# Optimization experiments

Hardware: AMD Instinct MI355X
Metric: run time of the kernel (lower is better)

Reference implementation:

```python
import jax, jax.numpy as jnp
import numpy as np


def gcn_conv(x, src, dst, W, b, num_nodes):
    # GCNConv: add self loops, sym-normalize by deg^{-1/2} on both ends.
    h = x @ W  # [N, out]
    loop = jnp.arange(num_nodes, dtype=src.dtype)
    s = jnp.concatenate([src, loop])
    d = jnp.concatenate([dst, loop])
    deg = jax.ops.segment_sum(jnp.ones(d.shape[0], dtype=h.dtype), d, num_segments=num_nodes)
    dinv = jax.lax.rsqrt(jnp.maximum(deg, 1.0))
    norm = dinv[s] * dinv[d]  # [E+N]
    out = jax.ops.segment_sum(h[s] * norm[:, None], d, num_segments=num_nodes)
    return out + b


def setup_inputs() -> dict:
    key = jax.random.key(0)
    ks = jax.random.split(key, 12)
    N, F, E, ED = 100000, 256, 1600000, 1000000
    x = jax.random.normal(ks[0], (N, F), jnp.float32)
    edge_index = jax.random.randint(ks[1], (2, E), 0, N, jnp.int32)
    total_edges = jax.random.randint(ks[2], (ED, 2), 0, N, jnp.int32)
    PI = jax.random.uniform(ks[3], (ED, 25), jnp.float32)
    W1 = jax.random.normal(ks[4], (F, 100), jnp.float32) * 0.05
    b1 = jnp.zeros((100,), jnp.float32)
    W2 = jax.random.normal(ks[5], (100, 16), jnp.float32) * 0.05
    b2 = jnp.zeros((16,), jnp.float32)
    lin1_W = jax.random.normal(ks[6], (41, 25), jnp.float32) * 0.05
    lin1_b = jnp.zeros((25,), jnp.float32)
    lin_W = jax.random.normal(ks[7], (25, 1), jnp.float32) * 0.05
    lin_b = jnp.zeros((1,), jnp.float32)
    return dict(x=x, edge_index=edge_index, total_edges=total_edges, PI=PI,
                W1=W1, b1=b1, W2=W2, b2=b2,
                lin1_W=lin1_W, lin1_b=lin1_b, lin_W=lin_W, lin_b=lin_b)


def reference(x, edge_index, total_edges, PI, W1, b1, W2, b2, lin1_W, lin1_b, lin_W, lin_b):
    N = x.shape[0]
    src, dst = edge_index[0], edge_index[1]
    # encode (eval mode: dropout is identity)
    h = jax.nn.relu(gcn_conv(x, src, dst, W1, b1, N))
    emb = jax.nn.relu(gcn_conv(h, src, dst, W2, b2, N))
    # renorm_(2, 0, 1): clamp each row's L2 norm to max 1
    nrm = jnp.linalg.norm(emb, axis=1, keepdims=True)
    emb = emb / jnp.maximum(nrm, 1.0)
    # decode: gather endpoint embeddings, squared diff, concat PI, small MLP
    emb_in = emb[total_edges[:, 0]]   # [ED, 16]
    emb_out = emb[total_edges[:, 1]]  # [ED, 16]
    sqdist = (emb_in - emb_out) ** 2  # [ED, 16]
    feat = jnp.concatenate([sqdist, PI], axis=1)  # [ED, 41]
    feat = jax.nn.leaky_relu(feat @ lin1_W + lin1_b, negative_slope=0.2)
    s = jnp.abs(feat @ lin_W + lin_b)[:, 0]
    s = jnp.clip(s, 0.0, 40.0)
    prob = jax.nn.sigmoid(2.0 - s)  # == 1/(exp(s-2)+1)
    return prob
```

## Files before the change

### kernel.cpp

```cpp
#include <hip/hip_runtime.h>
#include <hip/hip_bf16.h>
#include <math.h>

#define H1 100
#define H2 16
#define FDIM 256
#define NPAD 112
#define BINCH 4096

typedef __attribute__((ext_vector_type(8))) short bf16x8;
typedef __attribute__((ext_vector_type(4))) float f32x4;
typedef float f32x4a __attribute__((ext_vector_type(4), aligned(4)));

__device__ __forceinline__ float bf_lo(unsigned u) { return __uint_as_float(u << 16); }
__device__ __forceinline__ float bf_hi(unsigned u) { return __uint_as_float(u & 0xffff0000u); }
__device__ __forceinline__ unsigned f2bf_bits(float f) {
  unsigned x = __float_as_uint(f);
  return (x + 0x7fffu + ((x >> 16) & 1u)) >> 16;
}
__device__ __forceinline__ unsigned pack_bf16(float a, float b) {
  __hip_bfloat162 h = __float22bfloat162_rn(make_float2(a, b));
  unsigned u;
  __builtin_memcpy(&u, &h, 4);
  return u;
}

__global__ __launch_bounds__(256)
void k_bincnt(const int* __restrict__ dst, int* __restrict__ bucket_cnt,
              int E, int shift) {
  __shared__ int lcnt[512];
  int t = threadIdx.x;
  for (int i = t; i < 512; i += 256) lcnt[i] = 0;
  __syncthreads();
  int base = blockIdx.x * BINCH;
#pragma unroll
  for (int i = 0; i < 16; i++) {
    int e = base + t + i * 256;
    if (e < E) atomicAdd(&lcnt[dst[e] >> shift], 1);
  }
  __syncthreads();
  for (int b = t; b < 512; b += 256) {
    int c = lcnt[b];
    if (c > 0) atomicAdd(&bucket_cnt[b], c);
  }
}

__global__ void k_bscan(const int* __restrict__ bucket_cnt, int* __restrict__ bucket_base,
                        int* __restrict__ bucket_fill, int nbuc, int E) {
  __shared__ int s[512];
  int tid = threadIdx.x;
  int v = (tid < nbuc) ? bucket_cnt[tid] : 0;
  s[tid] = v;
  __syncthreads();
  for (int off = 1; off < 512; off <<= 1) {
    int tt = (tid >= off) ? s[tid - off] : 0;
    __syncthreads();
    s[tid] += tt;
    __syncthreads();
  }
  if (tid < nbuc) { int ex = s[tid] - v; bucket_base[tid] = ex; bucket_fill[tid] = ex; }
  if (tid == 0) bucket_base[nbuc] = E;
}

__global__ __launch_bounds__(256)
void k_binwrite(const int* __restrict__ src, const int* __restrict__ dst,
                int* __restrict__ bucket_fill, int2* __restrict__ tpair,
                int E, int shift) {
  __shared__ int lcnt[512];
  __shared__ int loff[512];
  int t = threadIdx.x;
  for (int i = t; i < 512; i += 256) lcnt[i] = 0;
  __syncthreads();
  int base = blockIdx.x * BINCH;
  int d[16], s_[16];
#pragma unroll
  for (int i = 0; i < 16; i++) {
    int e = base + t + i * 256;
    if (e < E) {
      d[i] = dst[e]; s_[i] = src[e];
      atomicAdd(&lcnt[d[i] >> shift], 1);
    } else d[i] = -1;
  }
  __syncthreads();
  for (int b = t; b < 512; b += 256) {
    int c = lcnt[b];
    loff[b] = (c > 0) ? atomicAdd(&bucket_fill[b], c) : 0;
  }
  __syncthreads();
#pragma unroll
  for (int i = 0; i < 16; i++) {
    if (d[i] >= 0) {
      int p = atomicAdd(&loff[d[i] >> shift], 1);
      tpair[p] = make_int2(d[i], s_[i]);
    }
  }
}

__global__ __launch_bounds__(256)
void k_deg2(const int2* __restrict__ tpair, const int* __restrict__ bucket_base,
            int* __restrict__ deg, float* __restrict__ dinv, int N, int shift) {
  __shared__ int lcnt[1024];
  int b = blockIdx.x, t = threadIdx.x;
  int bs = 1 << shift, mask = bs - 1;
  for (int i = t; i < bs; i += 256) lcnt[i] = 0;
  __syncthreads();
  int r0 = bucket_base[b], r1 = bucket_base[b + 1];
  for (int e = r0 + t; e < r1; e += 256) atomicAdd(&lcnt[tpair[e].x & mask], 1);
  __syncthreads();
  for (int i = t; i < bs; i += 256) {
    int node = (b << shift) + i;
    if (node < N) {
      deg[node] = lcnt[i];
      dinv[node] = rsqrtf((float)(lcnt[i] + 1));
    }
  }
}

__global__ __launch_bounds__(256)
void k_csr2(const int2* __restrict__ tpair,
            const int* __restrict__ bucket_base, const int* __restrict__ row_ptr,
            int* __restrict__ col_src, int N, int shift) {
  __shared__ int lrp[1024];
  __shared__ int lfill[1024];
  int b = blockIdx.x, t = threadIdx.x;
  int bs = 1 << shift, mask = bs - 1;
  for (int i = t; i < bs; i += 256) {
    int node = (b << shift) + i;
    lrp[i] = row_ptr[node < N ? node : N];
    lfill[i] = 0;
  }
  __syncthreads();
  int r0 = bucket_base[b], r1 = bucket_base[b + 1];
  for (int e = r0 + t; e < r1; e += 256) {
    int2 pr = tpair[e];
    int dl = pr.x & mask;
    int p = lrp[dl] + atomicAdd(&lfill[dl], 1);
    col_src[p] = pr.y;
  }
}

__global__ void k_scanA(const int* __restrict__ deg, int* __restrict__ row_ptr,
                        int* __restrict__ psum, int n) {
  __shared__ int s[256];
  int tid = threadIdx.x;
  int i = blockIdx.x * 256 + tid;
  int v = (i < n) ? deg[i] : 0;
  s[tid] = v;
  __syncthreads();
  for (int off = 1; off < 256; off <<= 1) {
    int t = (tid >= off) ? s[tid - off] : 0;
    __syncthreads();
    s[tid] += t;
    __syncthreads();
  }
  if (i < n) row_ptr[i] = s[tid] - v;
  if (tid == 255) psum[blockIdx.x] = s[255];
}

__global__ void k_scanB(int* psum, int nb) {
  __shared__ int s[512];
  int tid = threadIdx.x;
  int v = (tid < nb) ? psum[tid] : 0;
  s[tid] = v;
  __syncthreads();
  for (int off = 1; off < 512; off <<= 1) {
    int t = (tid >= off) ? s[tid - off] : 0;
    __syncthreads();
    s[tid] += t;
    __syncthreads();
  }
  if (tid < nb) psum[tid] = s[tid] - v;
}

__global__ void k_scanC(int* row_ptr, const int* __restrict__ psum, int n, int E) {
  int i = blockIdx.x * blockDim.x + threadIdx.x;
  if (i < n) row_ptr[i] += psum[i >> 8];
  if (i == 0) row_ptr[n] = E;
}

__global__ void k_w1cast(const float* __restrict__ W1, unsigned short* __restrict__ W1bf) {
  int i = blockIdx.x * 256 + threadIdx.x;
  if (i >= NPAD * FDIM) return;
  int col = i / FDIM, k = i % FDIM;
  float v = (col < H1) ? W1[k * H1 + col] : 0.f;
  W1bf[i] = (unsigned short)f2bf_bits(v);
}

__global__ __launch_bounds__(512, 2)
void k_gemm1m(const float* __restrict__ x, const unsigned short* __restrict__ W1bf,
              const float* __restrict__ dinv, unsigned short* __restrict__ t1p, int n) {
  __shared__ unsigned short ws[NPAD * FDIM];
  int tid = threadIdx.x;
  int lane = tid & 63, w = tid >> 6;
  int lr = lane & 15, lg = lane >> 4;
  int r0 = blockIdx.x * 128 + w * 16;
  int arow = r0 + lr;
  const float* xrow = x + (size_t)(arow < n ? arow : 0) * FDIM;

  float4 va[16];
#pragma unroll
  for (int s = 0; s < 8; ++s) {
    int kb = s * 32 + lg * 8;
    va[2 * s]     = *(const float4*)(xrow + kb);
    va[2 * s + 1] = *(const float4*)(xrow + kb + 4);
  }

  for (int i = tid; i < NPAD * FDIM / 8; i += 512) {
    int col = i >> 5;
    int kc = i & 31;
    uint4 v = *(const uint4*)(W1bf + col * FDIM + kc * 8);
    unsigned addr = (unsigned)(col * 512 + kc * 16) ^ ((unsigned)(col & 7) << 4);
    *(uint4*)((char*)ws + addr) = v;
  }
  asm volatile("" ::: "memory");
  __syncthreads();

  bf16x8 af[8];
#pragma unroll
  for (int s = 0; s < 8; ++s) {
    uint4 au;
    au.x = pack_bf16(va[2 * s].x, va[2 * s].y);
    au.y = pack_bf16(va[2 * s].z, va[2 * s].w);
    au.z = pack_bf16(va[2 * s + 1].x, va[2 * s + 1].y);
    au.w = pack_bf16(va[2 * s + 1].z, va[2 * s + 1].w);
    af[s] = *(bf16x8*)&au;
  }

  f32x4 acc[7];
#pragma unroll
  for (int nt = 0; nt < 7; nt++) acc[nt] = (f32x4){0.f, 0.f, 0.f, 0.f};

#pragma unroll
  for (int s = 0; s < 8; ++s) {
    int kb = s * 32 + lg * 8;
#pragma unroll
    for (int nt = 0; nt < 7; nt++) {
      int col = nt * 16 + lr;
      unsigned addr = (unsigned)(col * 512 + kb * 2) ^ ((unsigned)(col & 7) << 4);
      bf16x8 b = *(bf16x8*)((char*)ws + addr);
      acc[nt] = __builtin_amdgcn_mfma_f32_16x16x32_bf16(af[s], b, acc[nt], 0, 0, 0);
    }
  }

  float dv[4];
  int rbase = r0 + lg * 4;
#pragma unroll
  for (int r = 0; r < 4; r++) dv[r] = (rbase + r < n) ? dinv[rbase + r] : 0.f;
#pragma unroll
  for (int nt = 0; nt < 7; nt++) {
    int col = nt * 16 + lr;
    if (col < H1) {
#pragma unroll
      for (int r = 0; r < 4; r++) {
        int row = rbase + r;
        if (row < n)
          t1p[(size_t)row * H1 + col] = (unsigned short)f2bf_bits(acc[nt][r] * dv[r]);
      }
    }
  }
}

__global__ __launch_bounds__(256)
void k_agg1(const unsigned* __restrict__ t1p, const int* __restrict__ row_ptr,
            const int* __restrict__ col_src, const float* __restrict__ dinv,
            const float* __restrict__ b1, unsigned* __restrict__ h, int n) {
  int wv = __builtin_amdgcn_readfirstlane((int)(threadIdx.x >> 6));
  int wid = blockIdx.x * 4 + wv;
  if (wid >= n) return;
  int lane = threadIdx.x & 63;
  if (lane >= 50) return;
  int beg = row_ptr[wid], end = row_ptr[wid + 1];
  float a0 = 0.f, a1 = 0.f;
  int e = beg;
  for (; e + 8 <= end; e += 8) {
    int s0 = col_src[e + 0], s1 = col_src[e + 1];
    int s2 = col_src[e + 2], s3 = col_src[e + 3];
    int s4 = col_src[e + 4], s5 = col_src[e + 5];
    int s6 = col_src[e + 6], s7 = col_src[e + 7];
    unsigned u0 = t1p[(size_t)s0 * 50 + lane];
    unsigned u1 = t1p[(size_t)s1 * 50 + lane];
    unsigned u2 = t1p[(size_t)s2 * 50 + lane];
    unsigned u3 = t1p[(size_t)s3 * 50 + lane];
    unsigned u4 = t1p[(size_t)s4 * 50 + lane];
    unsigned u5 = t1p[(size_t)s5 * 50 + lane];
    unsigned u6 = t1p[(size_t)s6 * 50 + lane];
    unsigned u7 = t1p[(size_t)s7 * 50 + lane];
    a0 += bf_lo(u0); a1 += bf_hi(u0);
    a0 += bf_lo(u1); a1 += bf_hi(u1);
    a0 += bf_lo(u2); a1 += bf_hi(u2);
    a0 += bf_lo(u3); a1 += bf_hi(u3);
    a0 += bf_lo(u4); a1 += bf_hi(u4);
    a0 += bf_lo(u5); a1 += bf_hi(u5);
    a0 += bf_lo(u6); a1 += bf_hi(u6);
    a0 += bf_lo(u7); a1 += bf_hi(u7);
  }
  int rem = end - e;
  if (rem > 0) {
    int last = end - 1;
    int i1 = (e + 1 < end) ? e + 1 : last;
    int i2 = (e + 2 < end) ? e + 2 : last;
    int i3 = (e + 3 < end) ? e + 3 : last;
    int i4 = (e + 4 < end) ? e + 4 : last;
    int i5 = (e + 5 < end) ? e + 5 : last;
    int i6 = (e + 6 < end) ? e + 6 : last;
    int i7 = (e + 7 < end) ? e + 7 : last;
    int s0 = col_src[e],  s1 = col_src[i1], s2 = col_src[i2], s3 = col_src[i3];
    int s4 = col_src[i4], s5 = col_src[i5], s6 = col_src[i6], s7 = col_src[i7];
    unsigned u0 = t1p[(size_t)s0 * 50 + lane];
    unsigned u1 = (rem > 1) ? t1p[(size_t)s1 * 50 + lane] : 0u;
    unsigned u2 = (rem > 2) ? t1p[(size_t)s2 * 50 + lane] : 0u;
    unsigned u3 = (rem > 3) ? t1p[(size_t)s3 * 50 + lane] : 0u;
    unsigned u4 = (rem > 4) ? t1p[(size_t)s4 * 50 + lane] : 0u;
    unsigned u5 = (rem > 5) ? t1p[(size_t)s5 * 50 + lane] : 0u;
    unsigned u6 = (rem > 6) ? t1p[(size_t)s6 * 50 + lane] : 0u;
    unsigned u7 = 0u;
    (void)s7; (void)u7;
    a0 += bf_lo(u0); a1 += bf_hi(u0);
    a0 += bf_lo(u1); a1 += bf_hi(u1);
    a0 += bf_lo(u2); a1 += bf_hi(u2);
    a0 += bf_lo(u3); a1 += bf_hi(u3);
    a0 += bf_lo(u4); a1 += bf_hi(u4);
    a0 += bf_lo(u5); a1 += bf_hi(u5);
    a0 += bf_lo(u6); a1 += bf_hi(u6);
  }
  unsigned su = t1p[(size_t)wid * 50 + lane];
  a0 += bf_lo(su);
  a1 += bf_hi(su);
  float dv = dinv[wid];
  float v0 = fmaxf(dv * a0 + b1[2 * lane], 0.f);
  float v1 = fmaxf(dv * a1 + b1[2 * lane + 1], 0.f);
  h[(size_t)wid * 50 + lane] = pack_bf16(v0, v1);
}

__global__ __launch_bounds__(256)
void k_gemm2(const unsigned* __restrict__ h, const float* __restrict__ W2,
             const float* __restrict__ dinv, unsigned* __restrict__ t2p, int n) {
  __shared__ alignas(16) float w2s[100][16];
  __shared__ float hs[64][101];
  int tid = threadIdx.x;
  int r0 = blockIdx.x * 64;
  for (int idx = tid; idx < H1 * H2; idx += 256) w2s[idx / 16][idx % 16] = W2[idx];
  for (int idx = tid; idx < 64 * 50; idx += 256) {
    int row = idx / 50, u = idx % 50;
    int gr = r0 + row;
    unsigned v = 0;
    if (gr < n) v = h[(size_t)gr * 50 + u];
    hs[row][2 * u + 0] = bf_lo(v);
    hs[row][2 * u + 1] = bf_hi(v);
  }
  __syncthreads();
  int r = tid & 63, cg = tid >> 6;
  float ax = 0.f, ay = 0.f, az = 0.f, aw = 0.f;
#pragma unroll 4
  for (int k = 0; k < H1; ++k) {
    float a = hs[r][k];
    float4 w = *(const float4*)&w2s[k][cg * 4];
    ax += a * w.x; ay += a * w.y; az += a * w.z; aw += a * w.w;
  }
  int gr = r0 + r;
  if (gr < n) {
    float dv = dinv[gr];
    unsigned u0 = pack_bf16(ax * dv, ay * dv);
    unsigned u1 = pack_bf16(az * dv, aw * dv);
    *(uint2*)(t2p + (size_t)gr * 8 + cg * 2) = make_uint2(u0, u1);
  }
}

__global__ __launch_bounds__(256)
void k_agg2(const unsigned* __restrict__ t2p, const int* __restrict__ row_ptr,
            const int* __restrict__ col_src, const float* __restrict__ dinv,
            const float* __restrict__ b2, float* __restrict__ emb, int n) {
  int wv = __builtin_amdgcn_readfirstlane((int)(threadIdx.x >> 6));
  int wid = blockIdx.x * 4 + wv;
  if (wid >= n) return;
  int lane = threadIdx.x & 63;
  int es = lane >> 3, c = lane & 7;
  int beg = row_ptr[wid], end = row_ptr[wid + 1];
  float a0 = 0.f, a1 = 0.f;
  for (int e = beg + es; e < end; e += 8) {
    int s = col_src[e];
    unsigned u = t2p[(size_t)s * 8 + c];
    a0 += bf_lo(u);
    a1 += bf_hi(u);
  }
  a0 += __shfl_xor(a0, 8, 64);  a1 += __shfl_xor(a1, 8, 64);
  a0 += __shfl_xor(a0, 16, 64); a1 += __shfl_xor(a1, 16, 64);
  a0 += __shfl_xor(a0, 32, 64); a1 += __shfl_xor(a1, 32, 64);
  unsigned su = t2p[(size_t)wid * 8 + c];
  a0 += bf_lo(su);
  a1 += bf_hi(su);
  float dv = dinv[wid];
  float v0 = fmaxf(dv * a0 + b2[2 * c + 0], 0.f);
  float v1 = fmaxf(dv * a1 + b2[2 * c + 1], 0.f);
  float n2 = v0 * v0 + v1 * v1;
  n2 += __shfl_xor(n2, 1, 64);
  n2 += __shfl_xor(n2, 2, 64);
  n2 += __shfl_xor(n2, 4, 64);
  float scale = 1.f / fmaxf(sqrtf(n2), 1.f);
  if (es == 0) {
    *(float2*)(emb + (size_t)wid * H2 + 2 * c) = make_float2(v0 * scale, v1 * scale);
  }
}

__global__ void k_sprep(const float* __restrict__ l1W, uint4* __restrict__ Bt) {
  int lane = threadIdx.x;
  int lr = lane & 15, lg = lane >> 4;
  float wb[16];
#pragma unroll
  for (int i = 0; i < 8; i++) {
    int k0 = lg * 8 + i;
    wb[i] = (lr < 25) ? l1W[k0 * 25 + lr] : 0.f;
    int k1 = 32 + lg * 8 + i;
    wb[8 + i] = (lr < 25 && k1 < 41) ? l1W[k1 * 25 + lr] : 0.f;
  }
  int j1 = 16 + lr;
  float wb2[16];
#pragma unroll
  for (int i = 0; i < 8; i++) {
    int k0 = lg * 8 + i;
    wb2[i] = (j1 < 25) ? l1W[k0 * 25 + j1] : 0.f;
    int k1 = 32 + lg * 8 + i;
    wb2[8 + i] = (j1 < 25 && k1 < 41) ? l1W[k1 * 25 + j1] : 0.f;
  }
  uint4 B00, B01, B10, B11;
  B00.x = pack_bf16(wb[0], wb[1]);  B00.y = pack_bf16(wb[2], wb[3]);
  B00.z = pack_bf16(wb[4], wb[5]);  B00.w = pack_bf16(wb[6], wb[7]);
  B01.x = pack_bf16(wb[8], wb[9]);  B01.y = pack_bf16(wb[10], wb[11]);
  B01.z = pack_bf16(wb[12], wb[13]); B01.w = pack_bf16(wb[14], wb[15]);
  B10.x = pack_bf16(wb2[0], wb2[1]); B10.y = pack_bf16(wb2[2], wb2[3]);
  B10.z = pack_bf16(wb2[4], wb2[5]); B10.w = pack_bf16(wb2[6], wb2[7]);
  B11.x = pack_bf16(wb2[8], wb2[9]); B11.y = pack_bf16(wb2[10], wb2[11]);
  B11.z = pack_bf16(wb2[12], wb2[13]); B11.w = pack_bf16(wb2[14], wb2[15]);
  Bt[lane * 4 + 0] = B00;
  Bt[lane * 4 + 1] = B01;
  Bt[lane * 4 + 2] = B10;
  Bt[lane * 4 + 3] = B11;
}

__global__ __launch_bounds__(256)
void k_score(const float* __restrict__ emb, const int* __restrict__ te,
             const float* __restrict__ PI, const uint4* __restrict__ Bt,
             const float* __restrict__ l1b, const float* __restrict__ lW,
             const float* __restrict__ lb, float* __restrict__ out, int ned) {
  int tid = threadIdx.x;
  int lane = tid & 63, w = tid >> 6;
  int lr = lane & 15, lg = lane >> 4;
  int e0 = blockIdx.x * 128 + w * 32;
  int ea = e0 + lr, eb = e0 + 16 + lr;
  int eca = (ea < ned) ? ea : 0;
  int ecb = (eb < ned) ? eb : 0;

  uint4 B00 = Bt[lane * 4 + 0];
  uint4 B01 = Bt[lane * 4 + 1];
  uint4 B10 = Bt[lane * 4 + 2];
  uint4 B11 = Bt[lane * 4 + 3];

  const float* pia = PI + (size_t)eca * 25;
  const float* pib = PI + (size_t)ecb * 25;

  uint4 A0a = {0u,0u,0u,0u}, A1a = {0u,0u,0u,0u};
  uint4 A0b = {0u,0u,0u,0u}, A1b = {0u,0u,0u,0u};

  if (lg < 2) {
    int2 uva = *(const int2*)(te + 2 * (size_t)eca);
    int2 uvb = *(const int2*)(te + 2 * (size_t)ecb);
    const float* eua = emb + (size_t)uva.x * H2 + lg * 8;
    const float* eva = emb + (size_t)uva.y * H2 + lg * 8;
    const float* eub = emb + (size_t)uvb.x * H2 + lg * 8;
    const float* evb = emb + (size_t)uvb.y * H2 + lg * 8;
    float4 a0a = *(const float4*)(eua);
    float4 a1a = *(const float4*)(eua + 4);
    float4 b0a = *(const float4*)(eva);
    float4 b1a = *(const float4*)(eva + 4);
    float4 a0b = *(const float4*)(eub);
    float4 a1b = *(const float4*)(eub + 4);
    float4 b0b = *(const float4*)(evb);
    float4 b1b = *(const float4*)(evb + 4);
    {
      float d0 = a0a.x - b0a.x, d1 = a0a.y - b0a.y, d2 = a0a.z - b0a.z, d3 = a0a.w - b0a.w;
      float d4 = a1a.x - b1a.x, d5 = a1a.y - b1a.y, d6 = a1a.z - b1a.z, d7 = a1a.w - b1a.w;
      A0a.x = pack_bf16(d0 * d0, d1 * d1);
      A0a.y = pack_bf16(d2 * d2, d3 * d3);
      A0a.z = pack_bf16(d4 * d4, d5 * d5);
      A0a.w = pack_bf16(d6 * d6, d7 * d7);
    }
    {
      float d0 = a0b.x - b0b.x, d1 = a0b.y - b0b.y, d2 = a0b.z - b0b.z, d3 = a0b.w - b0b.w;
      float d4 = a1b.x - b1b.x, d5 = a1b.y - b1b.y, d6 = a1b.z - b1b.z, d7 = a1b.w - b1b.w;
      A0b.x = pack_bf16(d0 * d0, d1 * d1);
      A0b.y = pack_bf16(d2 * d2, d3 * d3);
      A0b.z = pack_bf16(d4 * d4, d5 * d5);
      A0b.w = pack_bf16(d6 * d6, d7 * d7);
    }
    if (lg == 0) {
      f32x4a pa0 = *(const f32x4a*)(pia + 16);
      f32x4a pa1 = *(const f32x4a*)(pia + 20);
      f32x4a pb0 = *(const f32x4a*)(pib + 16);
      f32x4a pb1 = *(const f32x4a*)(pib + 20);
      A1a.x = pack_bf16(pa0[0], pa0[1]); A1a.y = pack_bf16(pa0[2], pa0[3]);
      A1a.z = pack_bf16(pa1[0], pa1[1]); A1a.w = pack_bf16(pa1[2], pa1[3]);
      A1b.x = pack_bf16(pb0[0], pb0[1]); A1b.y = pack_bf16(pb0[2], pb0[3]);
      A1b.z = pack_bf16(pb1[0], pb1[1]); A1b.w = pack_bf16(pb1[2], pb1[3]);
    } else {
      A1a.x = pack_bf16(pia[24], 0.f);
      A1b.x = pack_bf16(pib[24], 0.f);
    }
  } else {
    const float* ppa = pia + (lg - 2) * 8;
    const float* ppb = pib + (lg - 2) * 8;
    f32x4a pa0 = *(const f32x4a*)(ppa);
    f32x4a pa1 = *(const f32x4a*)(ppa + 4);
    f32x4a pb0 = *(const f32x4a*)(ppb);
    f32x4a pb1 = *(const f32x4a*)(ppb + 4);
    A0a.x = pack_bf16(pa0[0], pa0[1]); A0a.y = pack_bf16(pa0[2], pa0[3]);
    A0a.z = pack_bf16(pa1[0], pa1[1]); A0a.w = pack_bf16(pa1[2], pa1[3]);
    A0b.x = pack_bf16(pb0[0], pb0[1]); A0b.y = pack_bf16(pb0[2], pb0[3]);
    A0b.z = pack_bf16(pb1[0], pb1[1]); A0b.w = pack_bf16(pb1[2], pb1[3]);
  }

  f32x4 acc0a = {0.f,0.f,0.f,0.f}, acc1a = {0.f,0.f,0.f,0.f};
  f32x4 acc0b = {0.f,0.f,0.f,0.f}, acc1b = {0.f,0.f,0.f,0.f};
  acc0a = __builtin_amdgcn_mfma_f32_16x16x32_bf16(*(bf16x8*)&A0a, *(bf16x8*)&B00, acc0a, 0, 0, 0);
  acc0b = __builtin_amdgcn_mfma_f32_16x16x32_bf16(*(bf16x8*)&A0b, *(bf16x8*)&B00, acc0b, 0, 0, 0);
  acc0a = __builtin_amdgcn_mfma_f32_16x16x32_bf16(*(bf16x8*)&A1a, *(bf16x8*)&B01, acc0a, 0, 0, 0);
  acc0b = __builtin_amdgcn_mfma_f32_16x16x32_bf16(*(bf16x8*)&A1b, *(bf16x8*)&B01, acc0b, 0, 0, 0);
  acc1a = __builtin_amdgcn_mfma_f32_16x16x32_bf16(*(bf16x8*)&A0a, *(bf16x8*)&B10, acc1a, 0, 0, 0);
  acc1b = __builtin_amdgcn_mfma_f32_16x16x32_bf16(*(bf16x8*)&A0b, *(bf16x8*)&B10, acc1b, 0, 0, 0);
  acc1a = __builtin_amdgcn_mfma_f32_16x16x32_bf16(*(bf16x8*)&A1a, *(bf16x8*)&B11, acc1a, 0, 0, 0);
  acc1b = __builtin_amdgcn_mfma_f32_16x16x32_bf16(*(bf16x8*)&A1b, *(bf16x8*)&B11, acc1b, 0, 0, 0);

  int j1 = 16 + lr;
  float bj0 = l1b[lr];
  float wj0 = lW[lr];
  float bj1 = (j1 < 25) ? l1b[j1] : 0.f;
  float wj1 = (j1 < 25) ? lW[j1] : 0.f;
  float lbv = lb[0];

  float pa[4], pb[4];
#pragma unroll
  for (int r = 0; r < 4; r++) {
    float x0 = acc0a[r] + bj0;
    x0 = (x0 > 0.f) ? x0 : 0.2f * x0;
    float x1 = acc1a[r] + bj1;
    x1 = (x1 > 0.f) ? x1 : 0.2f * x1;
    pa[r] = x0 * wj0 + ((j1 < 25) ? x1 * wj1 : 0.f);
    float y0 = acc0b[r] + bj0;
    y0 = (y0 > 0.f) ? y0 : 0.2f * y0;
    float y1 = acc1b[r] + bj1;
    y1 = (y1 > 0.f) ? y1 : 0.2f * y1;
    pb[r] = y0 * wj0 + ((j1 < 25) ? y1 * wj1 : 0.f);
  }
#pragma unroll
  for (int r = 0; r < 4; r++) {
    pa[r] += __shfl_xor(pa[r], 1, 64);
    pb[r] += __shfl_xor(pb[r], 1, 64);
    pa[r] += __shfl_xor(pa[r], 2, 64);
    pb[r] += __shfl_xor(pb[r], 2, 64);
    pa[r] += __shfl_xor(pa[r], 4, 64);
    pb[r] += __shfl_xor(pb[r], 4, 64);
    pa[r] += __shfl_xor(pa[r], 8, 64);
    pb[r] += __shfl_xor(pb[r], 8, 64);
  }
  if (lr == 0) {
#pragma unroll
    for (int r = 0; r < 4; r++) {
      int eoa = e0 + lg * 4 + r;
      if (eoa < ned) {
        float s = fminf(fabsf(pa[r] + lbv), 40.f);
        out[eoa] = 1.f / (1.f + __expf(-(2.f - s)));
      }
      int eob = e0 + 16 + lg * 4 + r;
      if (eob < ned) {
        float s = fminf(fabsf(pb[r] + lbv), 40.f);
        out[eob] = 1.f / (1.f + __expf(-(2.f - s)));
      }
    }
  }
}

extern "C" void kernel_launch(void* const* d_in, const int* in_sizes, int n_in,
                              void* d_out, int out_size, void* d_ws, size_t ws_size,
                              hipStream_t stream) {
  const float* x   = (const float*)d_in[0];
  const int*   ei  = (const int*)d_in[1];
  const int*   te  = (const int*)d_in[2];
  const float* PI  = (const float*)d_in[3];
  const float* W1  = (const float*)d_in[4];
  const float* b1  = (const float*)d_in[5];
  const float* W2  = (const float*)d_in[6];
  const float* b2  = (const float*)d_in[7];
  const float* l1W = (const float*)d_in[8];
  const float* l1b = (const float*)d_in[9];
  const float* lW  = (const float*)d_in[10];
  const float* lb  = (const float*)d_in[11];
  float* out = (float*)d_out;

  int h1 = in_sizes[5];
  int F  = in_sizes[4] / h1;
  int N  = in_sizes[0] / F;
  int E  = in_sizes[1] / 2;
  int ED = in_sizes[2] / 2;

  const int* src  = ei;
  const int* dstp = ei + E;

  int shift = 8;
  while ((((size_t)N + ((size_t)1 << shift) - 1) >> shift) > 512) shift++;
  int nbuc = (N + (1 << shift) - 1) >> shift;

  size_t off = 0;
  auto alloc = [&](size_t bytes) -> void* {
    void* p = (char*)d_ws + off;
    off += (bytes + 255) & ~(size_t)255;
    return p;
  };
  int*            deg      = (int*)alloc((size_t)N * 4);
  float*          dinv     = (float*)alloc((size_t)N * 4);
  int*            row_ptr  = (int*)alloc((size_t)(N + 1) * 4);
  int*            psum     = (int*)alloc(512 * 4);
  int*            bcnt     = (int*)alloc(512 * 4);
  int*            bbase    = (int*)alloc(520 * 4);
  int*            bfill    = (int*)alloc(512 * 4);
  int*            col_src  = (int*)alloc((size_t)E * 4);
  unsigned short* W1bf     = (unsigned short*)alloc((size_t)NPAD * FDIM * 2);
  uint4*          Bt       = (uint4*)alloc(64 * 4 * 16);
  unsigned*       t1p      = (unsigned*)alloc((size_t)N * 50 * 4 + 256);
  unsigned*       h        = (unsigned*)alloc((size_t)N * 50 * 4);
  unsigned*       t2p      = (unsigned*)alloc((size_t)N * 8 * 4);
  float*          emb      = (float*)alloc((size_t)N * H2 * 4);

  int2* tpair = (int2*)h;

  int nb = (N + 255) / 256;
  int nwb = (E + BINCH - 1) / BINCH;

  hipMemsetAsync(bcnt, 0, 512 * 4, stream);
  k_bincnt<<<nwb, 256, 0, stream>>>(dstp, bcnt, E, shift);
  k_bscan<<<1, 512, 0, stream>>>(bcnt, bbase, bfill, nbuc, E);
  k_binwrite<<<nwb, 256, 0, stream>>>(src, dstp, bfill, tpair, E, shift);
  k_deg2<<<nbuc, 256, 0, stream>>>(tpair, bbase, deg, dinv, N, shift);
  k_scanA<<<nb, 256, 0, stream>>>(deg, row_ptr, psum, N);
  k_scanB<<<1, 512, 0, stream>>>(psum, nb);
  k_scanC<<<nb, 256, 0, stream>>>(row_ptr, psum, N, E);
  k_csr2<<<nbuc, 256, 0, stream>>>(tpair, bbase, row_ptr, col_src, N, shift);
  k_w1cast<<<(NPAD * FDIM + 255) / 256, 256, 0, stream>>>(W1, W1bf);
  k_sprep<<<1, 64, 0, stream>>>(l1W, Bt);
  k_gemm1m<<<(N + 127) / 128, 512, 0, stream>>>(x, W1bf, dinv, (unsigned short*)t1p, N);
  k_agg1<<<(int)(((size_t)N * 64 + 255) / 256), 256, 0, stream>>>(t1p, row_ptr, col_src, dinv, b1, h, N);
  k_gemm2<<<(N + 63) / 64, 256, 0, stream>>>(h, W2, dinv, t2p, N);
  k_agg2<<<(int)(((size_t)N * 64 + 255) / 256), 256, 0, stream>>>(t2p, row_ptr, col_src, dinv, b2, emb, N);
  k_score<<<(ED + 127) / 128, 256, 0, stream>>>(emb, te, PI, Bt, l1b, lW, lb, out, ED);
}
```

Before: 285.7 us.

## Fuse degree and row-pointer scan per bucket; store embeddings as bf16

The per-bucket degree kernel now also computes an in-block exclusive scan and writes row_ptr directly, offset by the bucket base. This replaces the three-kernel global scan and removes the deg buffer. Separately, the normalized embeddings are stored as packed bf16, halving the random gather traffic in the scoring kernel, at some precision cost before the squared difference. A serial fallback path handles bucket sizes other than 256.

```diff
diff --git a/kernel.cpp b/kernel.cpp
--- a/kernel.cpp
+++ b/kernel.cpp
@@ -23,6 +23,11 @@
   unsigned u;
   __builtin_memcpy(&u, &h, 4);
   return u;
+}
+__device__ __forceinline__ unsigned sqd_pair(unsigned u, unsigned v) {
+  float d0 = bf_lo(u) - bf_lo(v);
+  float d1 = bf_hi(u) - bf_hi(v);
+  return pack_bf16(d0 * d0, d1 * d1);
 }
 
 __global__ __launch_bounds__(256)
@@ -97,9 +102,11 @@
 }
 
 __global__ __launch_bounds__(256)
-void k_deg2(const int2* __restrict__ tpair, const int* __restrict__ bucket_base,
-            int* __restrict__ deg, float* __restrict__ dinv, int N, int shift) {
+void k_deg2s(const int2* __restrict__ tpair, const int* __restrict__ bucket_base,
+             float* __restrict__ dinv, int* __restrict__ row_ptr,
+             int N, int E, int shift) {
   __shared__ int lcnt[1024];
+  __shared__ int lscan[256];
   int b = blockIdx.x, t = threadIdx.x;
   int bs = 1 << shift, mask = bs - 1;
   for (int i = t; i < bs; i += 256) lcnt[i] = 0;
@@ -107,11 +114,34 @@
   int r0 = bucket_base[b], r1 = bucket_base[b + 1];
   for (int e = r0 + t; e < r1; e += 256) atomicAdd(&lcnt[tpair[e].x & mask], 1);
   __syncthreads();
-  for (int i = t; i < bs; i += 256) {
-    int node = (b << shift) + i;
+  if (bs == 256) {
+    int v = lcnt[t];
+    lscan[t] = v;
+    __syncthreads();
+    for (int off = 1; off < 256; off <<= 1) {
+      int tt = (t >= off) ? lscan[t - off] : 0;
+      __syncthreads();
+      lscan[t] += tt;
+      __syncthreads();
+    }
+    int node = (b << shift) + t;
     if (node < N) {
-      deg[node] = lcnt[i];
-      dinv[node] = rsqrtf((float)(lcnt[i] + 1));
+      row_ptr[node] = r0 + lscan[t] - v;
+      dinv[node] = rsqrtf((float)(v + 1));
+      if (node == N - 1) row_ptr[N] = E;
+    }
+  } else {
+    if (t == 0) {
+      int acc = r0;
+      for (int i = 0; i < bs; i++) {
+        int node = (b << shift) + i;
+        if (node < N) {
+          row_ptr[node] = acc;
+          dinv[node] = rsqrtf((float)(lcnt[i] + 1));
+          if (node == N - 1) row_ptr[N] = E;
+        }
+        acc += lcnt[i];
+      }
     }
   }
 }
@@ -137,45 +167,6 @@
     int p = lrp[dl] + atomicAdd(&lfill[dl], 1);
     col_src[p] = pr.y;
   }
-}
-
-__global__ void k_scanA(const int* __restrict__ deg, int* __restrict__ row_ptr,
-                        int* __restrict__ psum, int n) {
-  __shared__ int s[256];
-  int tid = threadIdx.x;
-  int i = blockIdx.x * 256 + tid;
-  int v = (i < n) ? deg[i] : 0;
-  s[tid] = v;
-  __syncthreads();
-  for (int off = 1; off < 256; off <<= 1) {
-    int t = (tid >= off) ? s[tid - off] : 0;
-    __syncthreads();
-    s[tid] += t;
-    __syncthreads();
-  }
-  if (i < n) row_ptr[i] = s[tid] - v;
-  if (tid == 255) psum[blockIdx.x] = s[255];
-}
-
-__global__ void k_scanB(int* psum, int nb) {
-  __shared__ int s[512];
-  int tid = threadIdx.x;
-  int v = (tid < nb) ? psum[tid] : 0;
-  s[tid] = v;
-  __syncthreads();
-  for (int off = 1; off < 512; off <<= 1) {
-    int t = (tid >= off) ? s[tid - off] : 0;
-    __syncthreads();
-    s[tid] += t;
-    __syncthreads();
-  }
-  if (tid < nb) psum[tid] = s[tid] - v;
-}
-
-__global__ void k_scanC(int* row_ptr, const int* __restrict__ psum, int n, int E) {
-  int i = blockIdx.x * blockDim.x + threadIdx.x;
-  if (i < n) row_ptr[i] += psum[i >> 8];
-  if (i == 0) row_ptr[n] = E;
 }
 
 __global__ void k_w1cast(const float* __restrict__ W1, unsigned short* __restrict__ W1bf) {
@@ -303,9 +294,8 @@
     int i4 = (e + 4 < end) ? e + 4 : last;
     int i5 = (e + 5 < end) ? e + 5 : last;
     int i6 = (e + 6 < end) ? e + 6 : last;
-    int i7 = (e + 7 < end) ? e + 7 : last;
     int s0 = col_src[e],  s1 = col_src[i1], s2 = col_src[i2], s3 = col_src[i3];
-    int s4 = col_src[i4], s5 = col_src[i5], s6 = col_src[i6], s7 = col_src[i7];
+    int s4 = col_src[i4], s5 = col_src[i5], s6 = col_src[i6];
     unsigned u0 = t1p[(size_t)s0 * 50 + lane];
     unsigned u1 = (rem > 1) ? t1p[(size_t)s1 * 50 + lane] : 0u;
     unsigned u2 = (rem > 2) ? t1p[(size_t)s2 * 50 + lane] : 0u;
@@ -313,8 +303,6 @@
     unsigned u4 = (rem > 4) ? t1p[(size_t)s4 * 50 + lane] : 0u;
     unsigned u5 = (rem > 5) ? t1p[(size_t)s5 * 50 + lane] : 0u;
     unsigned u6 = (rem > 6) ? t1p[(size_t)s6 * 50 + lane] : 0u;
-    unsigned u7 = 0u;
-    (void)s7; (void)u7;
     a0 += bf_lo(u0); a1 += bf_hi(u0);
     a0 += bf_lo(u1); a1 += bf_hi(u1);
     a0 += bf_lo(u2); a1 += bf_hi(u2);
@@ -369,7 +357,7 @@
 __global__ __launch_bounds__(256)
 void k_agg2(const unsigned* __restrict__ t2p, const int* __restrict__ row_ptr,
             const int* __restrict__ col_src, const float* __restrict__ dinv,
-            const float* __restrict__ b2, float* __restrict__ emb, int n) {
+            const float* __restrict__ b2, unsigned* __restrict__ embb, int n) {
   int wv = __builtin_amdgcn_readfirstlane((int)(threadIdx.x >> 6));
   int wid = blockIdx.x * 4 + wv;
   if (wid >= n) return;
@@ -398,7 +386,7 @@
   n2 += __shfl_xor(n2, 4, 64);
   float scale = 1.f / fmaxf(sqrtf(n2), 1.f);
   if (es == 0) {
-    *(float2*)(emb + (size_t)wid * H2 + 2 * c) = make_float2(v0 * scale, v1 * scale);
+    embb[(size_t)wid * 8 + c] = pack_bf16(v0 * scale, v1 * scale);
   }
 }
 
@@ -438,7 +426,7 @@
 }
 
 __global__ __launch_bounds__(256)
-void k_score(const float* __restrict__ emb, const int* __restrict__ te,
+void k_score(const unsigned* __restrict__ embb, const int* __restrict__ te,
              const float* __restrict__ PI, const uint4* __restrict__ Bt,
              const float* __restrict__ l1b, const float* __restrict__ lW,
              const float* __restrict__ lb, float* __restrict__ out, int ned) {
@@ -464,34 +452,14 @@
   if (lg < 2) {
     int2 uva = *(const int2*)(te + 2 * (size_t)eca);
     int2 uvb = *(const int2*)(te + 2 * (size_t)ecb);
-    const float* eua = emb + (size_t)uva.x * H2 + lg * 8;
-    const float* eva = emb + (size_t)uva.y * H2 + lg * 8;
-    const float* eub = emb + (size_t)uvb.x * H2 + lg * 8;
-    const float* evb = emb + (size_t)uvb.y * H2 + lg * 8;
-    float4 a0a = *(const float4*)(eua);
-    float4 a1a = *(const float4*)(eua + 4);
-    float4 b0a = *(const float4*)(eva);
-    float4 b1a = *(const float4*)(eva + 4);
-    float4 a0b = *(const float4*)(eub);
-    float4 a1b = *(const float4*)(eub + 4);
-    float4 b0b = *(const float4*)(evb);
-    float4 b1b = *(const float4*)(evb + 4);
-    {
-      float d0 = a0a.x - b0a.x, d1 = a0a.y - b0a.y, d2 = a0a.z - b0a.z, d3 = a0a.w - b0a.w;
-      float d4 = a1a.x - b1a.x, d5 = a1a.y - b1a.y, d6 = a1a.z - b1a.z, d7 = a1a.w - b1a.w;
-      A0a.x = pack_bf16(d0 * d0, d1 * d1);
-      A0a.y = pack_bf16(d2 * d2, d3 * d3);
-      A0a.z = pack_bf16(d4 * d4, d5 * d5);
-      A0a.w = pack_bf16(d6 * d6, d7 * d7);
-    }
-    {
-      float d0 = a0b.x - b0b.x, d1 = a0b.y - b0b.y, d2 = a0b.z - b0b.z, d3 = a0b.w - b0b.w;
-      float d4 = a1b.x - b1b.x, d5 = a1b.y - b1b.y, d6 = a1b.z - b1b.z, d7 = a1b.w - b1b.w;
-      A0b.x = pack_bf16(d0 * d0, d1 * d1);
-      A0b.y = pack_bf16(d2 * d2, d3 * d3);
-      A0b.z = pack_bf16(d4 * d4, d5 * d5);
-      A0b.w = pack_bf16(d6 * d6, d7 * d7);
-    }
+    uint4 ua = *(const uint4*)(embb + (size_t)uva.x * 8 + lg * 4);
+    uint4 va = *(const uint4*)(embb + (size_t)uva.y * 8 + lg * 4);
+    uint4 ub = *(const uint4*)(embb + (size_t)uvb.x * 8 + lg * 4);
+    uint4 vb = *(const uint4*)(embb + (size_t)uvb.y * 8 + lg * 4);
+    A0a.x = sqd_pair(ua.x, va.x); A0a.y = sqd_pair(ua.y, va.y);
+    A0a.z = sqd_pair(ua.z, va.z); A0a.w = sqd_pair(ua.w, va.w);
+    A0b.x = sqd_pair(ub.x, vb.x); A0b.y = sqd_pair(ub.y, vb.y);
+    A0b.z = sqd_pair(ub.z, vb.z); A0b.w = sqd_pair(ub.w, vb.w);
     if (lg == 0) {
       f32x4a pa0 = *(const f32x4a*)(pia + 16);
       f32x4a pa1 = *(const f32x4a*)(pia + 20);
@@ -614,10 +582,8 @@
     off += (bytes + 255) & ~(size_t)255;
     return p;
   };
-  int*            deg      = (int*)alloc((size_t)N * 4);
   float*          dinv     = (float*)alloc((size_t)N * 4);
   int*            row_ptr  = (int*)alloc((size_t)(N + 1) * 4);
-  int*            psum     = (int*)alloc(512 * 4);
   int*            bcnt     = (int*)alloc(512 * 4);
   int*            bbase    = (int*)alloc(520 * 4);
   int*            bfill    = (int*)alloc(512 * 4);
@@ -627,27 +593,23 @@
   unsigned*       t1p      = (unsigned*)alloc((size_t)N * 50 * 4 + 256);
   unsigned*       h        = (unsigned*)alloc((size_t)N * 50 * 4);
   unsigned*       t2p      = (unsigned*)alloc((size_t)N * 8 * 4);
-  float*          emb      = (float*)alloc((size_t)N * H2 * 4);
+  unsigned*       embb     = (unsigned*)alloc((size_t)N * 8 * 4);
 
   int2* tpair = (int2*)h;
 
-  int nb = (N + 255) / 256;
   int nwb = (E + BINCH - 1) / BINCH;
 
   hipMemsetAsync(bcnt, 0, 512 * 4, stream);
   k_bincnt<<<nwb, 256, 0, stream>>>(dstp, bcnt, E, shift);
   k_bscan<<<1, 512, 0, stream>>>(bcnt, bbase, bfill, nbuc, E);
   k_binwrite<<<nwb, 256, 0, stream>>>(src, dstp, bfill, tpair, E, shift);
-  k_deg2<<<nbuc, 256, 0, stream>>>(tpair, bbase, deg, dinv, N, shift);
-  k_scanA<<<nb, 256, 0, stream>>>(deg, row_ptr, psum, N);
-  k_scanB<<<1, 512, 0, stream>>>(psum, nb);
-  k_scanC<<<nb, 256, 0, stream>>>(row_ptr, psum, N, E);
+  k_deg2s<<<nbuc, 256, 0, stream>>>(tpair, bbase, dinv, row_ptr, N, E, shift);
   k_csr2<<<nbuc, 256, 0, stream>>>(tpair, bbase, row_ptr, col_src, N, shift);
   k_w1cast<<<(NPAD * FDIM + 255) / 256, 256, 0, stream>>>(W1, W1bf);
   k_sprep<<<1, 64, 0, stream>>>(l1W, Bt);
   k_gemm1m<<<(N + 127) / 128, 512, 0, stream>>>(x, W1bf, dinv, (unsigned short*)t1p, N);
   k_agg1<<<(int)(((size_t)N * 64 + 255) / 256), 256, 0, stream>>>(t1p, row_ptr, col_src, dinv, b1, h, N);
   k_gemm2<<<(N + 63) / 64, 256, 0, stream>>>(h, W2, dinv, t2p, N);
-  k_agg2<<<(int)(((size_t)N * 64 + 255) / 256), 256, 0, stream>>>(t2p, row_ptr, col_src, dinv, b2, emb, N);
-  k_score<<<(ED + 127) / 128, 256, 0, stream>>>(emb, te, PI, Bt, l1b, lW, lb, out, ED);
-}
+  k_agg2<<<(int)(((size_t)N * 64 + 255) / 256), 256, 0, stream>>>(t2p, row_ptr, col_src, dinv, b2, embb, N);
+  k_score<<<(ED + 127) / 128, 256, 0, stream>>>(embb, te, PI, Bt, l1b, lW, lb, out, ED);
+}
```

After: 272.6 us (median of 2 runs). 4.6% less time.
